# Performance work log

Measured on AMD Instinct MI355X. Metric: run time of the kernel, lower is better.

## Reference

```python
import jax, jax.numpy as jnp
import numpy as np

N_HIDDEN = 512
N_MEMORY = 128
BUDGET = 16
BATCH = 32768


def setup_inputs() -> dict:
    key = jax.random.key(0)
    ks = jax.random.split(key, 4)
    s1 = 1.0 / np.sqrt(N_HIDDEN + N_MEMORY)
    s2 = 1.0 / np.sqrt(2048)
    return {
        "x": jax.random.normal(ks[0], (BATCH, N_HIDDEN), dtype=jnp.float32),
        "W1": jax.random.normal(ks[1], (N_HIDDEN + N_MEMORY, 2048), dtype=jnp.float32) * s1,
        "b1": jnp.zeros((2048,), dtype=jnp.float32),
        "W2": jax.random.normal(ks[2], (2048, 2048), dtype=jnp.float32) * s2,
        "b2": jnp.zeros((2048,), dtype=jnp.float32),
        "W3": jax.random.normal(ks[3], (2048, N_HIDDEN + N_MEMORY + 2), dtype=jnp.float32) * s2,
        "b3": jnp.zeros((N_HIDDEN + N_MEMORY + 2,), dtype=jnp.float32),
    }


def reference(x, W1, b1, W2, b2, W3, b3):
    batch = x.shape[0]
    dtype = x.dtype

    memory = jnp.zeros((batch, N_MEMORY), dtype=dtype).at[:, 0].set(float(BUDGET))
    halted = jnp.zeros((batch,), dtype=bool)
    final_probs = jnp.zeros((batch,), dtype=dtype)
    n_iters = jnp.zeros((batch,), dtype=dtype)  # never updated in the original forward

    def mlp(inp):
        h = jax.nn.relu(inp @ W1 + b1)
        h = jax.nn.relu(h @ W2 + b2)
        return h @ W3 + b3

    def step(carry, _):
        x, mem, halted, fp = carry
        out = mlp(jnp.concatenate([x, mem], axis=-1))  # [B, 2+H+M]
        probs = out[:, 0]
        halt_val = out[:, 1]
        hidden_out = out[:, 2:2 + N_HIDDEN]
        mem_out = out[:, 2 + N_HIDDEN:]
        active = ~halted
        # torch compacts with boolean masks; masked-where is the dense equivalent
        x = jnp.where(active[:, None], hidden_out, x)
        mem = jnp.where(active[:, None], mem_out, mem)
        halt = jax.nn.sigmoid(halt_val) > 0.5  # sigmoid().round().bool()
        newly = active & halt
        fp = jnp.where(newly, probs, fp)
        halted = halted | newly
        return (x, mem, halted, fp), None

    (x, memory, halted, final_probs), _ = jax.lax.scan(
        step, (x, memory, halted, final_probs), None, length=BUDGET)

    return jax.nn.sigmoid(final_probs), n_iters
```

## Files before the change

kernel.cpp:

```cpp
#include <hip/hip_runtime.h>
#include <math.h>

typedef _Float16 f16;
typedef _Float16 f16x8 __attribute__((ext_vector_type(8)));
typedef float f32x4 __attribute__((ext_vector_type(4)));

#define NB 32768
#define NH 512
#define NM 128
#define NIN 640
#define NHID 2048
#define NOUT 642
#define NOUTP 768
#define ITERS 16
#define S1 2048.0f
#define EPS1 4.8828125e-4f

__device__ __forceinline__ void gload16(const void* g, void* lds) {
  __builtin_amdgcn_global_load_lds(
      reinterpret_cast<const __attribute__((address_space(1))) unsigned int*>((uintptr_t)g),
      reinterpret_cast<__attribute__((address_space(3))) unsigned int*>((unsigned int)(uintptr_t)lds),
      16, 0, 0);
}

__device__ __forceinline__ f32x4 mfma16(f16x8 a, f16x8 b, f32x4 c) {
  return __builtin_amdgcn_mfma_f32_16x16x32_f16(a, b, c, 0, 0, 0);
}

__device__ __forceinline__ void split2(float v, f16& a0, f16& a1) {
  a0 = (f16)v;
  a1 = (f16)((v - (float)a0) * S1);
}

__global__ void k_prepW(const float* __restrict__ W, f16* __restrict__ WT,
                        int K, int Nreal) {
  __shared__ float tile[32][33];
  int k0 = blockIdx.x * 32, n0 = blockIdx.y * 32;
  int tx = threadIdx.x & 31, ty = threadIdx.x >> 5;
#pragma unroll
  for (int r = 0; r < 4; ++r) {
    int kk = ty + 8 * r;
    int n = n0 + tx;
    tile[kk][tx] = (n < Nreal) ? W[(size_t)(k0 + kk) * Nreal + n] : 0.0f;
  }
  __syncthreads();
#pragma unroll
  for (int r = 0; r < 4; ++r) {
    int nl = ty + 8 * r;
    float v = tile[tx][nl];
    f16 a0, a1; split2(v, a0, a1);
    size_t o = (size_t)(n0 + nl) * (2 * K) + k0 + tx;
    WT[o] = a0; WT[o + K] = a1;
  }
}

__global__ void k_splitX(const float* __restrict__ x, f16* __restrict__ xm2) {
  int i = blockIdx.x * 256 + threadIdx.x;
  int row = i >> 9, c = i & 511;
  f16 a0, a1; split2(x[i], a0, a1);
  size_t o = (size_t)row * (2 * NIN) + c;
  xm2[o] = a0; xm2[o + NIN] = a1;
}

__global__ void k_init(f16* __restrict__ xm2, float* __restrict__ fpb,
                       int* __restrict__ list0, int* __restrict__ cnt) {
  int gid = blockIdx.x * blockDim.x + threadIdx.x;
  if (gid < NB * NM) {
    int row = gid >> 7, c = gid & 127;
    size_t o = (size_t)row * (2 * NIN) + 512 + c;
    xm2[o] = (f16)((c == 0) ? 16.0f : 0.0f);
    xm2[o + NIN] = (f16)0.0f;
  }
  if (gid < NB) { fpb[gid] = 0.0f; list0[gid] = gid; }
  if (gid < 32) cnt[gid] = (gid == 0) ? NB : 0;
}


#define GEMM_PREAMBLE()                                                     \
  int tid = threadIdx.x;                                                    \
  int w = tid >> 6, lane = tid & 63;                                        \
  int wr = w >> 1, wc = w & 1;                                              \
  int lm = lane & 15, kb = lane >> 4;                                       \
  int kidx = ((kb ^ ((lm >> 1) & 3)) << 3);                                 \
  int ksrc = (((tid & 3) ^ ((tid >> 3) & 3)) << 3);                         \
  int stg = tid * 8;                                                        \
  int afo[4], bfo[4];                                                       \
  _Pragma("unroll") for (int m = 0; m < 4; ++m)                             \
    afo[m] = (wr * 64 + m * 16 + lm) * 32 + kidx;                           \
  _Pragma("unroll") for (int n = 0; n < 4; ++n)                             \
    bfo[n] = (wc * 64 + n * 16 + lm) * 32 + kidx + 8192;                    \
  f32x4 acc0[4][4], acc1[4][4];                                             \
  _Pragma("unroll") for (int m = 0; m < 4; ++m)                             \
  _Pragma("unroll") for (int n = 0; n < 4; ++n) {                           \
    acc0[m][n] = (f32x4)0.0f; acc1[m][n] = (f32x4)0.0f;                     \
  }

#define GEMM_COMPUTE(BASE)                                                  \
  {                                                                         \
    const f16* _sb = (BASE);                                                \
    f16x8 fa0[4], fa1[4], fb0[4], fb1[4];                                   \
    _Pragma("unroll") for (int m = 0; m < 4; ++m) {                         \
      fa0[m] = *(const f16x8*)&_sb[afo[m]];                                 \
      fa1[m] = *(const f16x8*)&_sb[4096 + afo[m]];                          \
    }                                                                       \
    _Pragma("unroll") for (int n = 0; n < 4; ++n) {                         \
      fb0[n] = *(const f16x8*)&_sb[bfo[n]];                                 \
      fb1[n] = *(const f16x8*)&_sb[4096 + bfo[n]];                          \
    }                                                                       \
    __builtin_amdgcn_s_setprio(1);                                          \
    _Pragma("unroll") for (int m = 0; m < 4; ++m)                           \
    _Pragma("unroll") for (int n = 0; n < 4; ++n) {                         \
      acc0[m][n] = mfma16(fa0[m], fb0[n], acc0[m][n]);                      \
      acc1[m][n] = mfma16(fa0[m], fb1[n], acc1[m][n]);                      \
      acc1[m][n] = mfma16(fa1[m], fb0[n], acc1[m][n]);                      \
    }                                                                       \
    __builtin_amdgcn_s_setprio(0);                                          \
  }

#define STAGE8(K0, DST, PSA, PSB)                                           \
  {                                                                         \
    _Pragma("unroll") for (int s = 0; s < 2; ++s) {                         \
      gload16(pA + s * (PSA) + (K0), (DST) + s * 4096 + stg);               \
      gload16(pA2 + s * (PSA) + (K0), (DST) + 2048 + s * 4096 + stg);       \
    }                                                                       \
    _Pragma("unroll") for (int s = 0; s < 2; ++s) {                         \
      gload16(pB + s * (PSB) + (K0), (DST) + 8192 + s * 4096 + stg);        \
      gload16(pB2 + s * (PSB) + (K0), (DST) + 10240 + s * 4096 + stg);      \
    }                                                                       \
  }

#define GEMM_PIPELOOP(KTOT, PSA, PSB)                                       \
  STAGE8(0, &SB[0], PSA, PSB);                                              \
  __syncthreads();                                                          \
  {                                                                         \
    int pb = 0;                                                             \
    for (int k0 = 0; k0 < (KTOT); k0 += 32, pb ^= 1) {                      \
      if (k0 + 32 < (KTOT))                                                 \
        STAGE8(k0 + 32, pb ? &SB[0] : &SB[16384], PSA, PSB);                \
      GEMM_COMPUTE(pb ? &SB[16384] : &SB[0]);                               \
      __syncthreads();                                                      \
    }                                                                       \
  }

#define COMBINE(m, n, q) (acc0[m][n][q] + EPS1 * acc1[m][n][q])

#define MAP16(ID, BX, NY) int NY = ((ID) & 7) + 8 * (((ID) >> 3) & 1); int BX = (ID) >> 4;

__global__ __launch_bounds__(256, 2) void k_l1(
    const f16* __restrict__ xm2, const f16* __restrict__ WT,
    const float* __restrict__ b1, f16* __restrict__ h1,
    const int* __restrict__ list, const int* __restrict__ cntp,
    int chunk_off, int chunk_rows) {
  int cnt = *cntp;
  MAP16(blockIdx.x, bx, ny);
  int lm0 = bx * 128;
  if (chunk_off + lm0 >= cnt) return;
  int lim = cnt - chunk_off; if (lim > chunk_rows) lim = chunk_rows;
  int n0 = ny * 128;

  __shared__ f16 SB[2 * 16384];
  GEMM_PREAMBLE();

  int pu = chunk_off + lm0 + (tid >> 2);
  int pu2 = pu + 64;
  int idx = list[pu < cnt ? pu : (cnt - 1)];
  int idx2 = list[pu2 < cnt ? pu2 : (cnt - 1)];
  const f16* pA = xm2 + (size_t)idx * (2 * NIN) + ksrc;
  const f16* pA2 = xm2 + (size_t)idx2 * (2 * NIN) + ksrc;
  const f16* pB = WT + (size_t)(n0 + (tid >> 2)) * (2 * NIN) + ksrc;
  const f16* pB2 = pB + (size_t)64 * (2 * NIN);

  GEMM_PIPELOOP(NIN, NIN, NIN);

#pragma unroll
  for (int n = 0; n < 4; ++n) {
    int col = n0 + wc * 64 + n * 16 + lm;
    float bb = b1[col];
#pragma unroll
    for (int m = 0; m < 4; ++m) {
#pragma unroll
      for (int q = 0; q < 4; ++q) {
        int gr = lm0 + wr * 64 + m * 16 + kb * 4 + q;
        if (gr < lim) {
          float v = fmaxf(COMBINE(m, n, q) + bb, 0.0f);
          f16 a0, a1; split2(v, a0, a1);
          size_t o = (size_t)gr * (2 * NHID) + col;
          h1[o] = a0; h1[o + NHID] = a1;
        }
      }
    }
  }
}

__global__ __launch_bounds__(256, 2) void k_l2(
    const f16* __restrict__ h1, const f16* __restrict__ WT,
    const float* __restrict__ b2, f16* __restrict__ h2,
    const int* __restrict__ cntp, int chunk_off, int chunk_rows) {
  int cnt = *cntp;
  MAP16(blockIdx.x, bx, ny);
  int lm0 = bx * 128;
  if (chunk_off + lm0 >= cnt) return;
  int lim = cnt - chunk_off; if (lim > chunk_rows) lim = chunk_rows;
  int n0 = ny * 128;

  __shared__ f16 SB[2 * 16384];
  GEMM_PREAMBLE();

  const f16* pA = h1 + (size_t)(lm0 + (tid >> 2)) * (2 * NHID) + ksrc;
  const f16* pA2 = pA + (size_t)64 * (2 * NHID);
  const f16* pB = WT + (size_t)(n0 + (tid >> 2)) * (2 * NHID) + ksrc;
  const f16* pB2 = pB + (size_t)64 * (2 * NHID);

  GEMM_PIPELOOP(NHID, NHID, NHID);

#pragma unroll
  for (int n = 0; n < 4; ++n) {
    int col = n0 + wc * 64 + n * 16 + lm;
    float bb = b2[col];
#pragma unroll
    for (int m = 0; m < 4; ++m) {
#pragma unroll
      for (int q = 0; q < 4; ++q) {
        int gr = lm0 + wr * 64 + m * 16 + kb * 4 + q;
        if (gr < lim) {
          float v = fmaxf(COMBINE(m, n, q) + bb, 0.0f);
          f16 a0, a1; split2(v, a0, a1);
          size_t o = (size_t)gr * (2 * NHID) + col;
          h2[o] = a0; h2[o + NHID] = a1;
        }
      }
    }
  }
}

__global__ __launch_bounds__(256, 2) void k_l3(
    const f16* __restrict__ h2, const f16* __restrict__ WT,
    const float* __restrict__ b3, f16* __restrict__ xm2,
    float* __restrict__ fpb,
    const int* __restrict__ list, int* __restrict__ listn,
    const int* __restrict__ cntp, int* __restrict__ cntn,
    int chunk_off, int chunk_rows) {
  int cnt = *cntp;
  int id = blockIdx.x;
  int bx = id / 6, ny = id - bx * 6;
  int lm0 = bx * 128;
  if (chunk_off + lm0 >= cnt) return;
  int lim = cnt - chunk_off; if (lim > chunk_rows) lim = chunk_rows;
  int n0 = ny * 128;

  __shared__ f16 SB[2 * 16384];
  GEMM_PREAMBLE();

  const f16* pA = h2 + (size_t)(lm0 + (tid >> 2)) * (2 * NHID) + ksrc;
  const f16* pA2 = pA + (size_t)64 * (2 * NHID);
  const f16* pB = WT + (size_t)(n0 + (tid >> 2)) * (2 * NHID) + ksrc;
  const f16* pB2 = pB + (size_t)64 * (2 * NHID);

  GEMM_PIPELOOP(NHID, NHID, NHID);

  float* SBp = (float*)SB;
  float* SBh = (float*)SB + 128;

  float bb[4]; int colv[4];
#pragma unroll
  for (int n = 0; n < 4; ++n) {
    colv[n] = n0 + wc * 64 + n * 16 + lm;
    bb[n] = (colv[n] < NOUT) ? b3[colv[n]] : 0.0f;
  }
#pragma unroll
  for (int m = 0; m < 4; ++m) {
#pragma unroll
    for (int q = 0; q < 4; ++q) {
      int gr = lm0 + wr * 64 + m * 16 + kb * 4 + q;
      if (gr >= lim) continue;
      int r = list[chunk_off + gr];
#pragma unroll
      for (int n = 0; n < 4; ++n) {
        int col = colv[n];
        if (col >= NOUT) continue;
        float v = COMBINE(m, n, q) + bb[n];
        if (col == 0) {
          SBp[gr - lm0] = v;
        } else if (col == 1) {
          SBh[gr - lm0] = v;
        } else if (col < 2 + NH) {
          f16 a0, a1; split2(v, a0, a1);
          size_t o = (size_t)r * (2 * NIN) + (col - 2);
          xm2[o] = a0; xm2[o + NIN] = a1;
        } else {
          f16 a0, a1; split2(v, a0, a1);
          size_t o = (size_t)r * (2 * NIN) + 512 + (col - 2 - NH);
          xm2[o] = a0; xm2[o + NIN] = a1;
        }
      }
    }
  }

  if (ny == 0) {
    __syncthreads();
    int rcount = lim - lm0; if (rcount > 128) rcount = 128;
    if (tid < rcount) {
      int r = list[chunk_off + lm0 + tid];
      if (SBh[tid] > 0.0f) {
        fpb[r] = SBp[tid];
      } else {
        int pos = atomicAdd(cntn, 1);
        listn[pos] = r;
      }
    }
  }
}

__global__ void k_final(const float* __restrict__ fpb, float* __restrict__ out) {
  int i = blockIdx.x * blockDim.x + threadIdx.x;
  if (i < NB) {
    out[i] = 1.0f / (1.0f + expf(-fpb[i]));
    out[NB + i] = 0.0f;
  }
}

extern "C" void kernel_launch(void* const* d_in, const int* in_sizes, int n_in,
                              void* d_out, int out_size, void* d_ws, size_t ws_size,
                              hipStream_t stream) {
  const float* x  = (const float*)d_in[0];
  const float* W1 = (const float*)d_in[1];
  const float* b1 = (const float*)d_in[2];
  const float* W2 = (const float*)d_in[3];
  const float* b2 = (const float*)d_in[4];
  const float* W3 = (const float*)d_in[5];
  const float* b3 = (const float*)d_in[6];
  float* out = (float*)d_out;

  char* p = (char*)d_ws;
  auto alloc = [&](size_t bytes) {
    char* r = p;
    p += (bytes + 255) & ~(size_t)255;
    return r;
  };
  f16* xm2  = (f16*)alloc((size_t)NB * 2 * NIN * 2);
  f16* W1T  = (f16*)alloc((size_t)NHID * 2 * NIN * 2);
  f16* W2T  = (f16*)alloc((size_t)NHID * 2 * NHID * 2);
  f16* W3T  = (f16*)alloc((size_t)NOUTP * 2 * NHID * 2);
  float* fpb   = (float*)alloc((size_t)NB * 4);
  int* list0   = (int*)alloc((size_t)NB * 4);
  int* list1   = (int*)alloc((size_t)NB * 4);
  int* cnt     = (int*)alloc(32 * 4);

  size_t used = (size_t)(p - (char*)d_ws);
  size_t remain = (ws_size > used) ? (ws_size - used) : 0;
  long long chl = (long long)(remain / ((size_t)2 * 2 * NHID * 2));
  int CH = (int)(chl > NB ? NB : chl);
  CH &= ~127;
  if (CH > 8192) CH = 8192;
  if (CH < 128) CH = 128;
  f16* h1 = (f16*)alloc((size_t)CH * 2 * NHID * 2);
  f16* h2 = (f16*)alloc((size_t)CH * 2 * NHID * 2);
  int nchunks = (NB + CH - 1) / CH;

  k_prepW<<<dim3(NIN / 32, NHID / 32), 256, 0, stream>>>(W1, W1T, NIN, NHID);
  k_prepW<<<dim3(NHID / 32, NHID / 32), 256, 0, stream>>>(W2, W2T, NHID, NHID);
  k_prepW<<<dim3(NHID / 32, NOUTP / 32), 256, 0, stream>>>(W3, W3T, NHID, NOUT);
  k_splitX<<<(NB * NH) / 256, 256, 0, stream>>>(x, xm2);
  k_init<<<(NB * NM) / 256, 256, 0, stream>>>(xm2, fpb, list0, cnt);

  for (int t = 0; t < ITERS; ++t) {
    const int* lc = (t & 1) ? list1 : list0;
    int* ln       = (t & 1) ? list0 : list1;
    const int* cc = cnt + t;
    int* cn       = cnt + t + 1;
    for (int c = 0; c < nchunks; ++c) {
      int off = c * CH;
      int rows = NB - off; if (rows > CH) rows = CH;
      int g1 = (CH / 128) * 16;
      k_l1<<<g1, 256, 0, stream>>>(xm2, W1T, b1, h1, lc, cc, off, rows);
      k_l2<<<g1, 256, 0, stream>>>(h1, W2T, b2, h2, cc, off, rows);
      int g3 = (CH / 128) * 6;
      k_l3<<<g3, 256, 0, stream>>>(h2, W3T, b3, xm2, fpb, lc, ln, cc, cn, off, rows);
    }
  }
  k_final<<<NB / 256, 256, 0, stream>>>(fpb, out);
}
```

Baseline: 3.879 ms.

## Switch GEMMs to 32x32x16 MFMA and XCD-aware block mapping

Replaces the 16x16x32 f16 MFMA tiles with 32x32x16 MFMA across all three layer GEMMs. This changes the LDS fragment offsets, swizzle, accumulator layout and epilogue row mapping to match. The larger instruction means fewer MFMA issues and fragment loads per K step. Block-to-tile mapping is also changed to group row tiles per XCD for L2 reuse of the A operand. The risks are higher accumulator register pressure and possible mistakes in the new output row mapping.

Result: slower. 4.525 ms (+16.7%).

```diff
diff --git a/kernel.cpp b/kernel.cpp
--- a/kernel.cpp
+++ b/kernel.cpp
@@ -3,7 +3,7 @@
 
 typedef _Float16 f16;
 typedef _Float16 f16x8 __attribute__((ext_vector_type(8)));
-typedef float f32x4 __attribute__((ext_vector_type(4)));
+typedef float f32x16 __attribute__((ext_vector_type(16)));
 
 #define NB 32768
 #define NH 512
@@ -23,8 +23,8 @@
       16, 0, 0);
 }
 
-__device__ __forceinline__ f32x4 mfma16(f16x8 a, f16x8 b, f32x4 c) {
-  return __builtin_amdgcn_mfma_f32_16x16x32_f16(a, b, c, 0, 0, 0);
+__device__ __forceinline__ f32x16 mfma32(f16x8 a, f16x8 b, f32x16 c) {
+  return __builtin_amdgcn_mfma_f32_32x32x16_f16(a, b, c, 0, 0, 0);
 }
 
 __device__ __forceinline__ void split2(float v, f16& a0, f16& a1) {
@@ -80,41 +80,49 @@
   int tid = threadIdx.x;                                                    \
   int w = tid >> 6, lane = tid & 63;                                        \
   int wr = w >> 1, wc = w & 1;                                              \
-  int lm = lane & 15, kb = lane >> 4;                                       \
-  int kidx = ((kb ^ ((lm >> 1) & 3)) << 3);                                 \
+  int l31 = lane & 31, kg = lane >> 5;                                      \
   int ksrc = (((tid & 3) ^ ((tid >> 3) & 3)) << 3);                         \
   int stg = tid * 8;                                                        \
-  int afo[4], bfo[4];                                                       \
-  _Pragma("unroll") for (int m = 0; m < 4; ++m)                             \
-    afo[m] = (wr * 64 + m * 16 + lm) * 32 + kidx;                           \
-  _Pragma("unroll") for (int n = 0; n < 4; ++n)                             \
-    bfo[n] = (wc * 64 + n * 16 + lm) * 32 + kidx + 8192;                    \
-  f32x4 acc0[4][4], acc1[4][4];                                             \
-  _Pragma("unroll") for (int m = 0; m < 4; ++m)                             \
-  _Pragma("unroll") for (int n = 0; n < 4; ++n) {                           \
-    acc0[m][n] = (f32x4)0.0f; acc1[m][n] = (f32x4)0.0f;                     \
+  int afo[2][2], bfo[2][2];                                                 \
+  _Pragma("unroll") for (int mi = 0; mi < 2; ++mi)                          \
+  _Pragma("unroll") for (int ks = 0; ks < 2; ++ks) {                        \
+    int row = wr * 64 + mi * 32 + l31;                                      \
+    afo[mi][ks] = row * 32 + ((((ks << 1) + kg) ^ ((row >> 1) & 3)) << 3);  \
+  }                                                                         \
+  _Pragma("unroll") for (int ni = 0; ni < 2; ++ni)                          \
+  _Pragma("unroll") for (int ks = 0; ks < 2; ++ks) {                        \
+    int row = wc * 64 + ni * 32 + l31;                                      \
+    bfo[ni][ks] = 8192 + row * 32 +                                         \
+                  ((((ks << 1) + kg) ^ ((row >> 1) & 3)) << 3);             \
+  }                                                                         \
+  f32x16 acc0[2][2], acc1[2][2];                                            \
+  _Pragma("unroll") for (int mi = 0; mi < 2; ++mi)                          \
+  _Pragma("unroll") for (int ni = 0; ni < 2; ++ni) {                        \
+    acc0[mi][ni] = (f32x16)0.0f; acc1[mi][ni] = (f32x16)0.0f;               \
   }
 
 #define GEMM_COMPUTE(BASE)                                                  \
   {                                                                         \
     const f16* _sb = (BASE);                                                \
-    f16x8 fa0[4], fa1[4], fb0[4], fb1[4];                                   \
-    _Pragma("unroll") for (int m = 0; m < 4; ++m) {                         \
-      fa0[m] = *(const f16x8*)&_sb[afo[m]];                                 \
-      fa1[m] = *(const f16x8*)&_sb[4096 + afo[m]];                          \
+    _Pragma("unroll") for (int ks = 0; ks < 2; ++ks) {                      \
+      f16x8 fa0[2], fa1[2], fb0[2], fb1[2];                                 \
+      _Pragma("unroll") for (int mi = 0; mi < 2; ++mi) {                    \
+        fa0[mi] = *(const f16x8*)&_sb[afo[mi][ks]];                         \
+        fa1[mi] = *(const f16x8*)&_sb[4096 + afo[mi][ks]];                  \
+      }                                                                     \
+      _Pragma("unroll") for (int ni = 0; ni < 2; ++ni) {                    \
+        fb0[ni] = *(const f16x8*)&_sb[bfo[ni][ks]];                         \
+        fb1[ni] = *(const f16x8*)&_sb[4096 + bfo[ni][ks]];                  \
+      }                                                                     \
+      __builtin_amdgcn_s_setprio(1);                                        \
+      _Pragma("unroll") for (int mi = 0; mi < 2; ++mi)                      \
+      _Pragma("unroll") for (int ni = 0; ni < 2; ++ni) {                    \
+        acc0[mi][ni] = mfma32(fa0[mi], fb0[ni], acc0[mi][ni]);              \
+        acc1[mi][ni] = mfma32(fa0[mi], fb1[ni], acc1[mi][ni]);              \
+        acc1[mi][ni] = mfma32(fa1[mi], fb0[ni], acc1[mi][ni]);              \
+      }                                                                     \
+      __builtin_amdgcn_s_setprio(0);                                        \
     }                                                                       \
-    _Pragma("unroll") for (int n = 0; n < 4; ++n) {                         \
-      fb0[n] = *(const f16x8*)&_sb[bfo[n]];                                 \
-      fb1[n] = *(const f16x8*)&_sb[4096 + bfo[n]];                          \
-    }                                                                       \
-    __builtin_amdgcn_s_setprio(1);                                          \
-    _Pragma("unroll") for (int m = 0; m < 4; ++m)                           \
-    _Pragma("unroll") for (int n = 0; n < 4; ++n) {                         \
-      acc0[m][n] = mfma16(fa0[m], fb0[n], acc0[m][n]);                      \
-      acc1[m][n] = mfma16(fa0[m], fb1[n], acc1[m][n]);                      \
-      acc1[m][n] = mfma16(fa1[m], fb0[n], acc1[m][n]);                      \
-    }                                                                       \
-    __builtin_amdgcn_s_setprio(0);                                          \
   }
 
 #define STAGE8(K0, DST, PSA, PSB)                                           \
@@ -142,9 +150,14 @@
     }                                                                       \
   }
 
-#define COMBINE(m, n, q) (acc0[m][n][q] + EPS1 * acc1[m][n][q])
-
-#define MAP16(ID, BX, NY) int NY = ((ID) & 7) + 8 * (((ID) >> 3) & 1); int BX = (ID) >> 4;
+#define CROW(RG) (((RG) & 3) + 8 * ((RG) >> 2))
+
+#define MAPX(ID, NYT, NBX, BX, NY)                                          \
+  int BX, NY;                                                               \
+  if (((NBX) & 7) == 0) {                                                   \
+    int xcd = (ID) & 7, j = (ID) >> 3;                                      \
+    NY = j % (NYT); BX = xcd * ((NBX) >> 3) + j / (NYT);                    \
+  } else { BX = (ID) / (NYT); NY = (ID) % (NYT); }
 
 __global__ __launch_bounds__(256, 2) void k_l1(
     const f16* __restrict__ xm2, const f16* __restrict__ WT,
@@ -152,7 +165,8 @@
     const int* __restrict__ list, const int* __restrict__ cntp,
     int chunk_off, int chunk_rows) {
   int cnt = *cntp;
-  MAP16(blockIdx.x, bx, ny);
+  int nbx = gridDim.x >> 4;
+  MAPX(blockIdx.x, 16, nbx, bx, ny);
   int lm0 = bx * 128;
   if (chunk_off + lm0 >= cnt) return;
   int lim = cnt - chunk_off; if (lim > chunk_rows) lim = chunk_rows;
@@ -173,18 +187,18 @@
   GEMM_PIPELOOP(NIN, NIN, NIN);
 
 #pragma unroll
-  for (int n = 0; n < 4; ++n) {
-    int col = n0 + wc * 64 + n * 16 + lm;
+  for (int ni = 0; ni < 2; ++ni) {
+    int col = n0 + wc * 64 + ni * 32 + l31;
     float bb = b1[col];
 #pragma unroll
-    for (int m = 0; m < 4; ++m) {
-#pragma unroll
-      for (int q = 0; q < 4; ++q) {
-        int gr = lm0 + wr * 64 + m * 16 + kb * 4 + q;
-        if (gr < lim) {
-          float v = fmaxf(COMBINE(m, n, q) + bb, 0.0f);
+    for (int mi = 0; mi < 2; ++mi) {
+#pragma unroll
+      for (int rg = 0; rg < 16; ++rg) {
+        int grow = lm0 + wr * 64 + mi * 32 + CROW(rg) + 4 * kg;
+        if (grow < lim) {
+          float v = fmaxf(acc0[mi][ni][rg] + EPS1 * acc1[mi][ni][rg] + bb, 0.0f);
           f16 a0, a1; split2(v, a0, a1);
-          size_t o = (size_t)gr * (2 * NHID) + col;
+          size_t o = (size_t)grow * (2 * NHID) + col;
           h1[o] = a0; h1[o + NHID] = a1;
         }
       }
@@ -197,7 +211,8 @@
     const float* __restrict__ b2, f16* __restrict__ h2,
     const int* __restrict__ cntp, int chunk_off, int chunk_rows) {
   int cnt = *cntp;
-  MAP16(blockIdx.x, bx, ny);
+  int nbx = gridDim.x >> 4;
+  MAPX(blockIdx.x, 16, nbx, bx, ny);
   int lm0 = bx * 128;
   if (chunk_off + lm0 >= cnt) return;
   int lim = cnt - chunk_off; if (lim > chunk_rows) lim = chunk_rows;
@@ -214,18 +229,18 @@
   GEMM_PIPELOOP(NHID, NHID, NHID);
 
 #pragma unroll
-  for (int n = 0; n < 4; ++n) {
-    int col = n0 + wc * 64 + n * 16 + lm;
+  for (int ni = 0; ni < 2; ++ni) {
+    int col = n0 + wc * 64 + ni * 32 + l31;
     float bb = b2[col];
 #pragma unroll
-    for (int m = 0; m < 4; ++m) {
-#pragma unroll
-      for (int q = 0; q < 4; ++q) {
-        int gr = lm0 + wr * 64 + m * 16 + kb * 4 + q;
-        if (gr < lim) {
-          float v = fmaxf(COMBINE(m, n, q) + bb, 0.0f);
+    for (int mi = 0; mi < 2; ++mi) {
+#pragma unroll
+      for (int rg = 0; rg < 16; ++rg) {
+        int grow = lm0 + wr * 64 + mi * 32 + CROW(rg) + 4 * kg;
+        if (grow < lim) {
+          float v = fmaxf(acc0[mi][ni][rg] + EPS1 * acc1[mi][ni][rg] + bb, 0.0f);
           f16 a0, a1; split2(v, a0, a1);
-          size_t o = (size_t)gr * (2 * NHID) + col;
+          size_t o = (size_t)grow * (2 * NHID) + col;
           h2[o] = a0; h2[o + NHID] = a1;
         }
       }
@@ -241,8 +256,8 @@
     const int* __restrict__ cntp, int* __restrict__ cntn,
     int chunk_off, int chunk_rows) {
   int cnt = *cntp;
-  int id = blockIdx.x;
-  int bx = id / 6, ny = id - bx * 6;
+  int nbx = gridDim.x / 6;
+  MAPX(blockIdx.x, 6, nbx, bx, ny);
   int lm0 = bx * 128;
   if (chunk_off + lm0 >= cnt) return;
   int lim = cnt - chunk_off; if (lim > chunk_rows) lim = chunk_rows;
@@ -261,28 +276,23 @@
   float* SBp = (float*)SB;
   float* SBh = (float*)SB + 128;
 
-  float bb[4]; int colv[4];
-#pragma unroll
-  for (int n = 0; n < 4; ++n) {
-    colv[n] = n0 + wc * 64 + n * 16 + lm;
-    bb[n] = (colv[n] < NOUT) ? b3[colv[n]] : 0.0f;
-  }
-#pragma unroll
-  for (int m = 0; m < 4; ++m) {
-#pragma unroll
-    for (int q = 0; q < 4; ++q) {
-      int gr = lm0 + wr * 64 + m * 16 + kb * 4 + q;
-      if (gr >= lim) continue;
-      int r = list[chunk_off + gr];
-#pragma unroll
-      for (int n = 0; n < 4; ++n) {
-        int col = colv[n];
-        if (col >= NOUT) continue;
-        float v = COMBINE(m, n, q) + bb[n];
+#pragma unroll
+  for (int ni = 0; ni < 2; ++ni) {
+    int col = n0 + wc * 64 + ni * 32 + l31;
+    float bb = (col < NOUT) ? b3[col] : 0.0f;
+    if (col >= NOUT) continue;
+#pragma unroll
+    for (int mi = 0; mi < 2; ++mi) {
+#pragma unroll
+      for (int rg = 0; rg < 16; ++rg) {
+        int grow = lm0 + wr * 64 + mi * 32 + CROW(rg) + 4 * kg;
+        if (grow >= lim) continue;
+        int r = list[chunk_off + grow];
+        float v = acc0[mi][ni][rg] + EPS1 * acc1[mi][ni][rg] + bb;
         if (col == 0) {
-          SBp[gr - lm0] = v;
+          SBp[grow - lm0] = v;
         } else if (col == 1) {
-          SBh[gr - lm0] = v;
+          SBh[grow - lm0] = v;
         } else if (col < 2 + NH) {
           f16 a0, a1; split2(v, a0, a1);
           size_t o = (size_t)r * (2 * NIN) + (col - 2);
```
